# Kernel optimization log

Measured on AMD Instinct MI355X. Metric: run time of the kernel, lower is better.

## Reference

```python
import jax, jax.numpy as jnp
import numpy as np

WS = (7, 7, 7)          # window size (S, H, W)
NUM_HEADS = 6
DIM = 192
B_, NW = 128, 32        # total windows, windows per image (mask dim)
N = WS[0] * WS[1] * WS[2]  # 343 tokens per window


def _relative_position_index():
    # Faithful replica of the torch __init__ logic (incl. indexing='xy' and
    # the 3*W1-1 / 2*W1-1 multipliers).
    cs = np.arange(WS[0]); ch = np.arange(WS[1]); cw = np.arange(WS[2])
    coords = np.stack(np.meshgrid(cs, ch, cw, indexing='xy'))  # (3, Wh, Ws, Ww)
    cf = coords.reshape(3, -1)                                  # (3, N)
    rel = cf[:, :, None] - cf[:, None, :]                       # (3, N, N)
    rel = rel.transpose(1, 2, 0).astype(np.int64)               # (N, N, 3)
    rel[:, :, 0] += WS[0] - 1
    rel[:, :, 1] += WS[1] - 1
    rel[:, :, 2] += WS[2] - 1
    rel[:, :, 0] *= 3 * WS[1] - 1
    rel[:, :, 1] *= 2 * WS[1] - 1
    return rel.sum(-1)                                          # (N, N) int


def setup_inputs() -> dict:
    key = jax.random.key(0)
    ks = jax.random.split(key, 6)
    C = DIM
    x = jax.random.normal(ks[0], (B_, N, C), dtype=jnp.float32)
    mask = jax.random.normal(ks[1], (NW, N, N), dtype=jnp.float32)
    qkv_w = jax.random.normal(ks[2], (3 * C, C), dtype=jnp.float32) * 0.02
    qkv_b = jnp.zeros((3 * C,), dtype=jnp.float32)
    proj_w = jax.random.normal(ks[3], (C, C), dtype=jnp.float32) * 0.02
    proj_b = jnp.zeros((C,), dtype=jnp.float32)
    table_len = (2 * WS[0] - 1) * (2 * WS[1] - 1) * (2 * WS[2] - 1)
    rpb_table = jax.random.normal(ks[4], (table_len, NUM_HEADS), dtype=jnp.float32) * 0.02
    rel_index = jnp.asarray(_relative_position_index(), dtype=jnp.int32)
    return {"x": x, "mask": mask, "qkv_w": qkv_w, "qkv_b": qkv_b,
            "proj_w": proj_w, "proj_b": proj_b, "rpb_table": rpb_table,
            "rel_index": rel_index}


def reference(x, mask, qkv_w, qkv_b, proj_w, proj_b, rpb_table, rel_index):
    B, n, C = x.shape
    H = NUM_HEADS
    hd = C // H
    scale = hd ** (-0.5)
    qkv = x @ qkv_w.T + qkv_b                      # (B, N, 3C)
    qkv = qkv.reshape(B, n, 3, H, hd).transpose(2, 0, 3, 1, 4)  # (3, B, H, N, hd)
    q, k, v = qkv[0] * scale, qkv[1], qkv[2]
    attn = jnp.einsum('bhnd,bhmd->bhnm', q, k)     # (B, H, N, N)
    bias = rpb_table[rel_index.reshape(-1)].reshape(n, n, H)
    attn = attn + bias.transpose(2, 0, 1)[None]    # (B, H, N, N)
    nW = mask.shape[0]
    attn = attn.reshape(B // nW, nW, H, n, n) + mask[None, :, None]
    attn = jax.nn.softmax(attn.reshape(B, H, n, n), axis=-1)
    out = jnp.einsum('bhnm,bhmd->bhnd', attn, v)   # (B, H, N, hd)
    out = out.transpose(0, 2, 1, 3).reshape(B, n, C)
    return out @ proj_w.T + proj_b
```

## Files before the change

### kernel.cpp

```cpp
#include <hip/hip_runtime.h>
#include <hip/hip_fp16.h>
#include <hip/hip_bf16.h>
#include <stdint.h>

#define WN 343
#define NH 6
#define HD 32
#define CD 192
#define NB 128
#define NWM 32
#define BMROW 352
#define BMSLICE (11*16*BMROW)
#define BMKC (16*BMROW)
#define LOG2E 1.4426950408889634f
#define XTS 2064

typedef __attribute__((ext_vector_type(8))) short short8;
typedef __attribute__((ext_vector_type(4))) float f32x4;

__device__ __forceinline__ unsigned short f2bf(float f) {
  union { float f; uint32_t u; } v; v.f = f;
  uint32_t r = v.u + 0x7fffu + ((v.u >> 16) & 1u);
  return (unsigned short)(r >> 16);
}

__device__ __forceinline__ uint32_t pk2bf(float a, float b) {
  __hip_bfloat162 h = __float22bfloat162_rn(make_float2(a, b));
  return *(uint32_t*)&h;
}

__device__ __forceinline__ uint32_t pkh2(float a, float b) {
  __half2 h; h.x = __float2half(a); h.y = __float2half(b);
  return *(uint32_t*)&h;
}

typedef const __attribute__((address_space(1))) unsigned int* gas_ptr;
typedef __attribute__((address_space(3))) unsigned int* las_ptr;
__device__ __forceinline__ void gload16(const unsigned short* g, unsigned short* l) {
  __builtin_amdgcn_global_load_lds((gas_ptr)(const void*)g, (las_ptr)(void*)l, 16, 0, 0);
}

__device__ __forceinline__ void pipe_bar() {
  asm volatile("s_waitcnt vmcnt(0) lgkmcnt(0)" ::: "memory");
  __builtin_amdgcn_sched_barrier(0);
  __builtin_amdgcn_s_barrier();
  __builtin_amdgcn_sched_barrier(0);
}

__global__ __launch_bounds__(256) void prep_kernel(
    const float* __restrict__ wq, const float* __restrict__ wp,
    unsigned short* __restrict__ wqb, unsigned short* __restrict__ wpb,
    const int* __restrict__ rel, const float* __restrict__ rpb,
    const float* __restrict__ mask, uint32_t* __restrict__ bP,
    uint32_t* __restrict__ mP) {
  __shared__ float M[88][33];
  const int bid = blockIdx.x;
  const int tid = threadIdx.x;
  if (bid < 264) {
    const int h = bid / 44;
    const int rem = bid - h * 44;
    const int kc = rem >> 2;
    const int g = rem & 3;
    const int n0 = g * 88;
    const int k0 = kc * 32;
    for (int idx = tid; idx < 88 * 32; idx += 256) {
      int nl = idx >> 5, k = idx & 31;
      int n = n0 + nl;
      int nc = (n < WN) ? n : (WN - 1);
      M[nl][k] = (k0 + k < WN) ? rpb[rel[nc * WN + k0 + k] * NH + h] * LOG2E
                               : -30000.0f;
    }
    __syncthreads();
    uint32_t* outp = bP + (size_t)h * BMSLICE + (size_t)kc * BMKC;
    if (tid < 88) {
      const int nl = tid;
      const int n = n0 + nl;
#pragma unroll
      for (int quad = 0; quad < 4; ++quad) {
        uint4 o;
        o.x = pkh2(M[nl][quad * 8 + 0], M[nl][quad * 8 + 4]);
        o.y = pkh2(M[nl][quad * 8 + 1], M[nl][quad * 8 + 5]);
        o.z = pkh2(M[nl][quad * 8 + 2], M[nl][quad * 8 + 6]);
        o.w = pkh2(M[nl][quad * 8 + 3], M[nl][quad * 8 + 7]);
        *(uint4*)(outp + ((size_t)quad * 352 + n) * 4) = o;
      }
    }
    return;
  }
  int cb = bid - 264;
  if (cb < 352) {
    const int wdx = cb / 11;
    const int kc = cb - wdx * 11;
    const int k0 = kc * 32;
    const float* mw = mask + (size_t)wdx * (WN * WN);
    uint32_t* outp = mP + (size_t)wdx * BMSLICE + (size_t)kc * BMKC;
#pragma unroll
    for (int quad = 0; quad < 4; ++quad) {
      const int q8 = quad * 8;
#pragma unroll
      for (int j = 0; j < 2; ++j) {
        int n = tid + 256 * j;
        if (n < 352) {
          float v[8];
#pragma unroll
          for (int i = 0; i < 8; ++i) {
            int kk = k0 + q8 + i;
            v[i] = (n < WN && kk < WN) ? mw[n * WN + kk] * LOG2E : 0.0f;
          }
          uint4 o;
          o.x = pkh2(v[0], v[4]);
          o.y = pkh2(v[1], v[5]);
          o.z = pkh2(v[2], v[6]);
          o.w = pkh2(v[3], v[7]);
          *(uint4*)(outp + ((size_t)quad * 352 + n) * 4) = o;
        }
      }
    }
    return;
  }
  cb -= 352;
  if (cb < 54) {
    int g = cb * 256 + tid;
    int sk = g / 768; int rem = g - sk * 768;
    int row = rem >> 2; int cc = rem & 3;
    int s = sk / 6; int kt = sk - s * 6;
    int lch = cc ^ ((row >> 1) & 3);
    const float* src = wq + (size_t)(s * 192 + row) * CD + kt * 32 + lch * 8;
    f32x4 a = *(const f32x4*)src;
    f32x4 b = *(const f32x4*)(src + 4);
    union { short8 v8; uint32_t d[4]; } pk;
    pk.d[0] = pk2bf(a[0], a[1]);
    pk.d[1] = pk2bf(a[2], a[3]);
    pk.d[2] = pk2bf(b[0], b[1]);
    pk.d[3] = pk2bf(b[2], b[3]);
    *(short8*)(wqb + (size_t)g * 8) = pk.v8;
    return;
  }
  cb -= 54;
  int g = cb * 256 + tid;
  int kt = g / 768; int rem = g - kt * 768;
  int row = rem >> 2; int cc = rem & 3;
  int lch = cc ^ ((row >> 1) & 3);
  const float* src = wp + (size_t)row * CD + kt * 32 + lch * 8;
  f32x4 a = *(const f32x4*)src;
  f32x4 b = *(const f32x4*)(src + 4);
  union { short8 v8; uint32_t d[4]; } pk;
  pk.d[0] = pk2bf(a[0], a[1]);
  pk.d[1] = pk2bf(a[2], a[3]);
  pk.d[2] = pk2bf(b[0], b[1]);
  pk.d[3] = pk2bf(b[2], b[3]);
  *(short8*)(wpb + (size_t)g * 8) = pk.v8;
}

__global__ __launch_bounds__(256) void qkv_kernel(
    const float* __restrict__ x, const unsigned short* __restrict__ wqb,
    const float* __restrict__ bvec,
    unsigned short* __restrict__ qb, unsigned short* __restrict__ kb,
    unsigned short* __restrict__ vb) {
  __shared__ __align__(16) unsigned short SL[6 * XTS + 2 * 6144];
  unsigned short* B0 = SL + 6 * XTS;
  unsigned short* B1 = B0 + 6144;
  const int tid = threadIdx.x;
  const int wave = tid >> 6, lane = tid & 63;
  const int quad = lane >> 4, c = lane & 15;
  const int m0 = blockIdx.x * 64;
  const int chk = (quad ^ ((c >> 1) & 3)) * 8;

  auto WSTAGE = [&](unsigned short* buf, int s, int kt) {
    const unsigned short* gw = wqb + ((size_t)s * 6 + kt) * 6144 + tid * 8;
    unsigned short* lw = buf + (size_t)wave * 512;
    gload16(gw, lw);
    gload16(gw + 2048, lw + 2048);
    gload16(gw + 4096, lw + 4096);
  };

  WSTAGE(B0, 0, 0);
#pragma unroll
  for (int it = 0; it < 6; ++it) {
    int u = tid + 256 * it;
    int lrow = u / 24, c24 = u - lrow * 24;
    int kt = c24 >> 2, j = c24 & 3;
    const float* src = x + (size_t)(m0 + lrow) * CD + kt * 32 + j * 8;
    f32x4 a = *(const f32x4*)src;
    f32x4 b = *(const f32x4*)(src + 4);
    union { short8 v8; uint32_t d[4]; } pk;
    pk.d[0] = pk2bf(a[0], a[1]);
    pk.d[1] = pk2bf(a[2], a[3]);
    pk.d[2] = pk2bf(b[0], b[1]);
    pk.d[3] = pk2bf(b[2], b[3]);
    int cw = (j ^ ((lrow >> 1) & 3)) * 8;
    *(short8*)&SL[kt * XTS + lrow * 32 + cw] = pk.v8;
  }
  pipe_bar();

  const float qscale = 0.25503486f;
  f32x4 acc[12];
  unsigned short* Lh0 = B0;
  unsigned short* Lh1 = B0 + 2304;

  for (int s = 0; s < 3; ++s) {
#pragma unroll
    for (int j = 0; j < 12; ++j) acc[j] = (f32x4){0.f, 0.f, 0.f, 0.f};

    for (int kt = 0; kt < 6; ++kt) {
      unsigned short* cur = (kt & 1) ? B1 : B0;
      unsigned short* nxt = (kt & 1) ? B0 : B1;
      if (kt < 5) WSTAGE(nxt, s, kt + 1);
      const unsigned short* XLb = SL + kt * XTS;
      short8 af = *(const short8*)&XLb[(wave * 16 + c) * 32 + chk];
#pragma unroll
      for (int j = 0; j < 12; ++j) {
        short8 bfr = *(const short8*)&cur[(j * 16 + c) * 32 + chk];
        acc[j] = __builtin_amdgcn_mfma_f32_16x16x32_bf16(af, bfr, acc[j], 0, 0, 0);
      }
      pipe_bar();
    }

    unsigned short* dst = (s == 0) ? qb : ((s == 1) ? kb : vb);
    const float scl = (s == 0) ? qscale : 1.0f;
    const int n0 = s * 192;
    for (int hh = 0; hh < 3; ++hh) {
      __syncthreads();
#pragma unroll
      for (int jj = 0; jj < 4; ++jj) {
        int j = hh * 4 + jj;
        int hl = jj >> 1;
        int dd = (jj & 1) * 16 + c;
        float bn = bvec[n0 + j * 16 + c];
        unsigned short* L = hl ? Lh1 : Lh0;
#pragma unroll
        for (int r = 0; r < 4; ++r) {
          int m = wave * 16 + quad * 4 + r;
          L[m * 36 + dd] = f2bf((acc[j][r] + bn) * scl);
        }
      }
      __syncthreads();
      const int m = tid & 63;
      const int hl = (tid >> 6) & 1;
      const int half = tid >> 7;
      const int M = m0 + m;
      const int b = M / WN;
      const int tok = M - b * WN;
      const int h = hh * 2 + hl;
      const unsigned short* L = hl ? Lh1 : Lh0;
      unsigned short* drow = dst + (((size_t)b * NH + h) * WN + tok) * HD + half * 16;
      *(short8*)&drow[0] = *(const short8*)&L[m * 36 + half * 16];
      *(short8*)&drow[8] = *(const short8*)&L[m * 36 + half * 16 + 8];
    }
    if (s < 2) {
      __syncthreads();
      WSTAGE(B0, s + 1, 0);
      pipe_bar();
    }
  }
}

__global__ __launch_bounds__(512) void attn_kernel(
    const unsigned short* __restrict__ qb, const unsigned short* __restrict__ kb,
    const unsigned short* __restrict__ vb, const uint32_t* __restrict__ biasP,
    const uint32_t* __restrict__ maskP, unsigned short* __restrict__ ob) {
  __shared__ __align__(16) unsigned short Ks[352][40];
  __shared__ __align__(16) unsigned short Vt[HD][360];
  const int bid = blockIdx.x;
  const int job = (bid & 7) * 96 + (bid >> 3);
  const int wdx = job / 24;
  const int inner = job - wdx * 24;
  const int h = inner >> 2;
  const int b = (inner & 3) * 32 + wdx;
  const int tid = threadIdx.x;
  const int wave = tid >> 6, lane = tid & 63;
  const int quad = lane >> 4, c = lane & 15;
  const size_t base = ((size_t)b * NH + h) * (WN * HD);
  const unsigned short* q = qb + base;
  const unsigned short* k = kb + base;
  const unsigned short* v = vb + base;
  const uint32_t* bS = biasP + (size_t)h * BMSLICE;
  const uint32_t* mS = maskP + (size_t)wdx * BMSLICE;

  for (int t = tid; t < WN * 4; t += 512) {
    int r = t >> 2, ch = t & 3;
    int kk = r & 31;
    int row = (r & ~31) + 16 * ((kk >> 2) & 1) + 4 * (kk >> 3) + (kk & 3);
    *(short8*)&Ks[row][ch * 8] = *(const short8*)(k + r * HD + ch * 8);
  }
  for (int t = tid; t < 9 * 32; t += 512) {
    int kg = WN + (t >> 5);
    int kk = kg & 31;
    int row = (kg & ~31) + 16 * ((kk >> 2) & 1) + 4 * (kk >> 3) + (kk & 3);
    Ks[row][t & 31] = 0;
  }
  for (int t = tid; t < WN; t += 512) {
#pragma unroll
    for (int ch = 0; ch < 4; ++ch) {
      short8 vv = *(const short8*)(v + t * HD + ch * 8);
#pragma unroll
      for (int j = 0; j < 8; ++j) Vt[ch * 8 + j][t] = vv[j];
    }
  }
  for (int t = tid; t < 9 * 32; t += 512) {
    Vt[t & 31][WN + (t >> 5)] = 0;
  }
  __syncthreads();

  union { short8 v8; uint32_t d[4]; } on;
  on.d[0] = on.d[1] = on.d[2] = on.d[3] = 0x3F803F80u;

  for (int qt = wave; qt < 22; qt += 8) {
    const int q0 = qt * 16;
    int qr = q0 + c; if (qr > WN - 1) qr = WN - 1;
    const short8 qf = *(const short8*)(q + qr * HD + quad * 8);
    const uint32_t* bPtr = bS + ((size_t)quad * 352 + q0 + c) * 4;
    const uint32_t* mPtr = mS + ((size_t)quad * 352 + q0 + c) * 4;

    f32x4 o0 = (f32x4){0.f, 0.f, 0.f, 0.f};
    f32x4 o1 = (f32x4){0.f, 0.f, 0.f, 0.f};
    f32x4 accl = (f32x4){0.f, 0.f, 0.f, 0.f};
    uint4 bw = *(const uint4*)bPtr;
    uint4 mw = *(const uint4*)mPtr;
#pragma unroll 1
    for (int kc = 0; kc < 11; ++kc) {
      bPtr += BMKC; mPtr += BMKC;
      uint4 bwN = *(const uint4*)bPtr;
      uint4 mwN = *(const uint4*)mPtr;
      f32x4 cc0, cc1;
      {
        __half2 s2; float2 f;
        s2 = __hadd2(*(__half2*)&bw.x, *(__half2*)&mw.x);
        f = __half22float2(s2); cc0[0] = f.x; cc1[0] = f.y;
        s2 = __hadd2(*(__half2*)&bw.y, *(__half2*)&mw.y);
        f = __half22float2(s2); cc0[1] = f.x; cc1[1] = f.y;
        s2 = __hadd2(*(__half2*)&bw.z, *(__half2*)&mw.z);
        f = __half22float2(s2); cc0[2] = f.x; cc1[2] = f.y;
        s2 = __hadd2(*(__half2*)&bw.w, *(__half2*)&mw.w);
        f = __half22float2(s2); cc0[3] = f.x; cc1[3] = f.y;
      }
      const int k0 = kc * 32;
      short8 kf0 = *(const short8*)&Ks[k0 + c][quad * 8];
      short8 kf1 = *(const short8*)&Ks[k0 + 16 + c][quad * 8];
      __builtin_amdgcn_s_setprio(1);
      f32x4 s0 = __builtin_amdgcn_mfma_f32_16x16x32_bf16(kf0, qf, cc0, 0, 0, 0);
      f32x4 s1 = __builtin_amdgcn_mfma_f32_16x16x32_bf16(kf1, qf, cc1, 0, 0, 0);
      __builtin_amdgcn_s_setprio(0);
      float p0 = __builtin_amdgcn_exp2f(s0[0]), p1 = __builtin_amdgcn_exp2f(s0[1]);
      float p2 = __builtin_amdgcn_exp2f(s0[2]), p3 = __builtin_amdgcn_exp2f(s0[3]);
      float p4 = __builtin_amdgcn_exp2f(s1[0]), p5 = __builtin_amdgcn_exp2f(s1[1]);
      float p6 = __builtin_amdgcn_exp2f(s1[2]), p7 = __builtin_amdgcn_exp2f(s1[3]);
      union { short8 v8; uint32_t d[4]; } pf;
      pf.d[0] = pk2bf(p0, p1);
      pf.d[1] = pk2bf(p2, p3);
      pf.d[2] = pk2bf(p4, p5);
      pf.d[3] = pk2bf(p6, p7);
      short8 vf0 = *(const short8*)&Vt[c][k0 + quad * 8];
      short8 vf1 = *(const short8*)&Vt[16 + c][k0 + quad * 8];
      __builtin_amdgcn_s_setprio(1);
      o0 = __builtin_amdgcn_mfma_f32_16x16x32_bf16(pf.v8, vf0, o0, 0, 0, 0);
      o1 = __builtin_amdgcn_mfma_f32_16x16x32_bf16(pf.v8, vf1, o1, 0, 0, 0);
      accl = __builtin_amdgcn_mfma_f32_16x16x32_bf16(pf.v8, on.v8, accl, 0, 0, 0);
      __builtin_amdgcn_s_setprio(0);
      bw = bwN; mw = mwN;
    }

#pragma unroll
    for (int r = 0; r < 4; ++r) {
      int n = q0 + quad * 4 + r;
      if (n < WN) {
        float inv = 1.0f / accl[r];
        int M = b * WN + n;
        int rloc = M & 127;
        int xr2 = (rloc >> 1) & 3;
        size_t base2 = (((size_t)(M >> 7) * 6 + h) << 12) + rloc * 32;
        ob[base2 + (((c >> 3) ^ xr2) << 3) + (c & 7)] = f2bf(o0[r] * inv);
        ob[base2 + ((((c >> 3) | 2) ^ xr2) << 3) + (c & 7)] = f2bf(o1[r] * inv);
      }
    }
  }
}

__global__ __launch_bounds__(256) void proj_kernel(
    const unsigned short* __restrict__ obp, const unsigned short* __restrict__ wpb,
    const float* __restrict__ bvec, float* __restrict__ out) {
  __shared__ __align__(16) unsigned short SL[16384];
  const int tid = threadIdx.x;
  const int wave = tid >> 6, lane = tid & 63;
  const int quad = lane >> 4, c = lane & 15;
  const int m0 = blockIdx.x * 64;
  const int mb = blockIdx.x >> 1;
  const int r0 = (blockIdx.x & 1) * 64;
  const int chk = (quad ^ ((c >> 1) & 3)) * 8;

  f32x4 acc[12];
#pragma unroll
  for (int j = 0; j < 12; ++j) acc[j] = (f32x4){0.f, 0.f, 0.f, 0.f};

  auto STAGE = [&](unsigned short* buf, int kt) {
    const unsigned short* gx =
        obp + (((size_t)mb * 6 + kt) << 12) + r0 * 32 + tid * 8;
    const unsigned short* gw = wpb + (size_t)kt * 6144 + tid * 8;
    unsigned short* lx = buf + (size_t)wave * 512;
    unsigned short* lw = buf + 2048 + (size_t)wave * 512;
    gload16(gx, lx);
    gload16(gw, lw);
    gload16(gw + 2048, lw + 2048);
    gload16(gw + 4096, lw + 4096);
  };
  auto COMPUTE = [&](const unsigned short* buf) {
    const unsigned short* XLb = buf;
    const unsigned short* WLb = buf + 2048;
    short8 af = *(const short8*)&XLb[(wave * 16 + c) * 32 + chk];
#pragma unroll
    for (int j = 0; j < 12; ++j) {
      short8 bfr = *(const short8*)&WLb[(j * 16 + c) * 32 + chk];
      acc[j] = __builtin_amdgcn_mfma_f32_16x16x32_bf16(af, bfr, acc[j], 0, 0, 0);
    }
  };

  unsigned short* B0 = SL;
  unsigned short* B1 = SL + 8192;
  STAGE(B0, 0);
  pipe_bar();
#pragma unroll
  for (int p = 0; p < 3; ++p) {
    STAGE(B1, 2 * p + 1);
    COMPUTE(B0);
    pipe_bar();
    if (p < 2) STAGE(B0, 2 * p + 2);
    COMPUTE(B1);
    pipe_bar();
  }

#pragma unroll
  for (int j = 0; j < 12; ++j) {
    int col = j * 16 + c;
    float bn = bvec[col];
#pragma unroll
    for (int r = 0; r < 4; ++r) {
      int m = m0 + wave * 16 + quad * 4 + r;
      out[(size_t)m * CD + col] = acc[j][r] + bn;
    }
  }
}

extern "C" void kernel_launch(void* const* d_in, const int* in_sizes, int n_in,
                              void* d_out, int out_size, void* d_ws, size_t ws_size,
                              hipStream_t stream) {
  const float* x      = (const float*)d_in[0];
  const float* mask   = (const float*)d_in[1];
  const float* qkv_w  = (const float*)d_in[2];
  const float* qkv_b  = (const float*)d_in[3];
  const float* proj_w = (const float*)d_in[4];
  const float* proj_b = (const float*)d_in[5];
  const float* rpb    = (const float*)d_in[6];
  const int*   rel    = (const int*)d_in[7];
  float* out = (float*)d_out;

  char* ws = (char*)d_ws;
  uint32_t* biasP = (uint32_t*)ws;
  size_t off = 1486848;
  uint32_t* maskP = (uint32_t*)(ws + off); off += 7929856;
  unsigned short* qb = (unsigned short*)(ws + off); off += 16859136;
  unsigned short* kb = (unsigned short*)(ws + off); off += 16859136;
  unsigned short* vb = (unsigned short*)(ws + off); off += 16859136;
  unsigned short* wqb = (unsigned short*)(ws + off); off += 221184;
  unsigned short* wpb = (unsigned short*)(ws + off); off += 73728;
  unsigned short* obuf = (unsigned short*)(ws + off); off += 16859136;

  hipLaunchKernelGGL(prep_kernel, dim3(264 + 352 + 54 + 18), dim3(256),
                     0, stream,
                     qkv_w, proj_w, wqb, wpb, rel, rpb, mask, biasP, maskP);
  hipLaunchKernelGGL(qkv_kernel, dim3(686), dim3(256), 0, stream,
                     x, wqb, qkv_b, qb, kb, vb);
  hipLaunchKernelGGL(attn_kernel, dim3(NH * NB), dim3(512), 0, stream,
                     qb, kb, vb, biasP, maskP, obuf);
  hipLaunchKernelGGL(proj_kernel, dim3(686), dim3(256), 0, stream,
                     obuf, wpb, proj_b, out);
}
```

Measured before the change: 207.7 us.

## Fold bias, mask and proj-weight prep into the QKV GEMM launch

Splits the prep kernel so that only the QKV weight conversion runs first as a small kernel. The bias table, mask packing and projection weight conversion now run as extra blocks appended to the QKV GEMM grid, so they overlap with the GEMM instead of forming a serial stage. Mask block indices are also remapped so each group of eight consecutive blocks covers different windows. The cost is a larger combined kernel whose register and LDS budget is set by the GEMM path, applied to the prep blocks too.

```diff
diff --git a/kernel.cpp b/kernel.cpp
--- a/kernel.cpp
+++ b/kernel.cpp
@@ -47,18 +47,140 @@
   __builtin_amdgcn_sched_barrier(0);
 }
 
-__global__ __launch_bounds__(256) void prep_kernel(
-    const float* __restrict__ wq, const float* __restrict__ wp,
-    unsigned short* __restrict__ wqb, unsigned short* __restrict__ wpb,
+__global__ __launch_bounds__(256) void prep_w_kernel(
+    const float* __restrict__ wq, unsigned short* __restrict__ wqb) {
+  int g = blockIdx.x * 256 + threadIdx.x;
+  int sk = g / 768; int rem = g - sk * 768;
+  int row = rem >> 2; int cc = rem & 3;
+  int s = sk / 6; int kt = sk - s * 6;
+  int lch = cc ^ ((row >> 1) & 3);
+  const float* src = wq + (size_t)(s * 192 + row) * CD + kt * 32 + lch * 8;
+  f32x4 a = *(const f32x4*)src;
+  f32x4 b = *(const f32x4*)(src + 4);
+  union { short8 v8; uint32_t d[4]; } pk;
+  pk.d[0] = pk2bf(a[0], a[1]);
+  pk.d[1] = pk2bf(a[2], a[3]);
+  pk.d[2] = pk2bf(b[0], b[1]);
+  pk.d[3] = pk2bf(b[2], b[3]);
+  *(short8*)(wqb + (size_t)g * 8) = pk.v8;
+}
+
+__global__ __launch_bounds__(256) void qkv_kernel(
+    const float* __restrict__ x, const unsigned short* __restrict__ wqb,
+    const float* __restrict__ bvec,
+    unsigned short* __restrict__ qb, unsigned short* __restrict__ kb,
+    unsigned short* __restrict__ vb,
     const int* __restrict__ rel, const float* __restrict__ rpb,
     const float* __restrict__ mask, uint32_t* __restrict__ bP,
-    uint32_t* __restrict__ mP) {
-  __shared__ float M[88][33];
+    uint32_t* __restrict__ mP,
+    const float* __restrict__ wp, unsigned short* __restrict__ wpb) {
+  __shared__ __align__(16) unsigned short SL[6 * XTS + 2 * 6144];
   const int bid = blockIdx.x;
   const int tid = threadIdx.x;
-  if (bid < 264) {
-    const int h = bid / 44;
-    const int rem = bid - h * 44;
+
+  if (bid < 686) {
+    unsigned short* B0 = SL + 6 * XTS;
+    unsigned short* B1 = B0 + 6144;
+    const int wave = tid >> 6, lane = tid & 63;
+    const int quad = lane >> 4, c = lane & 15;
+    const int m0 = bid * 64;
+    const int chk = (quad ^ ((c >> 1) & 3)) * 8;
+
+    auto WSTAGE = [&](unsigned short* buf, int s, int kt) {
+      const unsigned short* gw = wqb + ((size_t)s * 6 + kt) * 6144 + tid * 8;
+      unsigned short* lw = buf + (size_t)wave * 512;
+      gload16(gw, lw);
+      gload16(gw + 2048, lw + 2048);
+      gload16(gw + 4096, lw + 4096);
+    };
+
+    WSTAGE(B0, 0, 0);
+#pragma unroll
+    for (int it = 0; it < 6; ++it) {
+      int u = tid + 256 * it;
+      int lrow = u / 24, c24 = u - lrow * 24;
+      int kt = c24 >> 2, j = c24 & 3;
+      const float* src = x + (size_t)(m0 + lrow) * CD + kt * 32 + j * 8;
+      f32x4 a = *(const f32x4*)src;
+      f32x4 b = *(const f32x4*)(src + 4);
+      union { short8 v8; uint32_t d[4]; } pk;
+      pk.d[0] = pk2bf(a[0], a[1]);
+      pk.d[1] = pk2bf(a[2], a[3]);
+      pk.d[2] = pk2bf(b[0], b[1]);
+      pk.d[3] = pk2bf(b[2], b[3]);
+      int cw = (j ^ ((lrow >> 1) & 3)) * 8;
+      *(short8*)&SL[kt * XTS + lrow * 32 + cw] = pk.v8;
+    }
+    pipe_bar();
+
+    const float qscale = 0.25503486f;
+    f32x4 acc[12];
+    unsigned short* Lh0 = B0;
+    unsigned short* Lh1 = B0 + 2304;
+
+    for (int s = 0; s < 3; ++s) {
+#pragma unroll
+      for (int j = 0; j < 12; ++j) acc[j] = (f32x4){0.f, 0.f, 0.f, 0.f};
+
+      for (int kt = 0; kt < 6; ++kt) {
+        unsigned short* cur = (kt & 1) ? B1 : B0;
+        unsigned short* nxt = (kt & 1) ? B0 : B1;
+        if (kt < 5) WSTAGE(nxt, s, kt + 1);
+        const unsigned short* XLb = SL + kt * XTS;
+        short8 af = *(const short8*)&XLb[(wave * 16 + c) * 32 + chk];
+#pragma unroll
+        for (int j = 0; j < 12; ++j) {
+          short8 bfr = *(const short8*)&cur[(j * 16 + c) * 32 + chk];
+          acc[j] = __builtin_amdgcn_mfma_f32_16x16x32_bf16(af, bfr, acc[j], 0, 0, 0);
+        }
+        pipe_bar();
+      }
+
+      unsigned short* dst = (s == 0) ? qb : ((s == 1) ? kb : vb);
+      const float scl = (s == 0) ? qscale : 1.0f;
+      const int n0 = s * 192;
+      for (int hh = 0; hh < 3; ++hh) {
+        __syncthreads();
+#pragma unroll
+        for (int jj = 0; jj < 4; ++jj) {
+          int j = hh * 4 + jj;
+          int hl = jj >> 1;
+          int dd = (jj & 1) * 16 + c;
+          float bn = bvec[n0 + j * 16 + c];
+          unsigned short* L = hl ? Lh1 : Lh0;
+#pragma unroll
+          for (int r = 0; r < 4; ++r) {
+            int m = wave * 16 + quad * 4 + r;
+            L[m * 36 + dd] = f2bf((acc[j][r] + bn) * scl);
+          }
+        }
+        __syncthreads();
+        const int m = tid & 63;
+        const int hl = (tid >> 6) & 1;
+        const int half = tid >> 7;
+        const int M = m0 + m;
+        const int b = M / WN;
+        const int tok = M - b * WN;
+        const int h = hh * 2 + hl;
+        const unsigned short* L = hl ? Lh1 : Lh0;
+        unsigned short* drow = dst + (((size_t)b * NH + h) * WN + tok) * HD + half * 16;
+        *(short8*)&drow[0] = *(const short8*)&L[m * 36 + half * 16];
+        *(short8*)&drow[8] = *(const short8*)&L[m * 36 + half * 16 + 8];
+      }
+      if (s < 2) {
+        __syncthreads();
+        WSTAGE(B0, s + 1, 0);
+        pipe_bar();
+      }
+    }
+    return;
+  }
+
+  int cb = bid - 686;
+  if (cb < 264) {
+    float (*M)[33] = (float (*)[33])&SL[0];
+    const int h = cb / 44;
+    const int rem = cb - h * 44;
     const int kc = rem >> 2;
     const int g = rem & 3;
     const int n0 = g * 88;
@@ -87,10 +209,12 @@
     }
     return;
   }
-  int cb = bid - 264;
+  cb -= 264;
   if (cb < 352) {
-    const int wdx = cb / 11;
-    const int kc = cb - wdx * 11;
+    const int g = bid & 7;
+    const int t = cb >> 3;
+    const int wdx = 4 * g + t / 11;
+    const int kc = t - 11 * (t / 11);
     const int k0 = kc * 32;
     const float* mw = mask + (size_t)wdx * (WN * WN);
     uint32_t* outp = mP + (size_t)wdx * BMSLICE + (size_t)kc * BMKC;
@@ -119,24 +243,6 @@
     return;
   }
   cb -= 352;
-  if (cb < 54) {
-    int g = cb * 256 + tid;
-    int sk = g / 768; int rem = g - sk * 768;
-    int row = rem >> 2; int cc = rem & 3;
-    int s = sk / 6; int kt = sk - s * 6;
-    int lch = cc ^ ((row >> 1) & 3);
-    const float* src = wq + (size_t)(s * 192 + row) * CD + kt * 32 + lch * 8;
-    f32x4 a = *(const f32x4*)src;
-    f32x4 b = *(const f32x4*)(src + 4);
-    union { short8 v8; uint32_t d[4]; } pk;
-    pk.d[0] = pk2bf(a[0], a[1]);
-    pk.d[1] = pk2bf(a[2], a[3]);
-    pk.d[2] = pk2bf(b[0], b[1]);
-    pk.d[3] = pk2bf(b[2], b[3]);
-    *(short8*)(wqb + (size_t)g * 8) = pk.v8;
-    return;
-  }
-  cb -= 54;
   int g = cb * 256 + tid;
   int kt = g / 768; int rem = g - kt * 768;
   int row = rem >> 2; int cc = rem & 3;
@@ -150,109 +256,6 @@
   pk.d[2] = pk2bf(b[0], b[1]);
   pk.d[3] = pk2bf(b[2], b[3]);
   *(short8*)(wpb + (size_t)g * 8) = pk.v8;
-}
-
-__global__ __launch_bounds__(256) void qkv_kernel(
-    const float* __restrict__ x, const unsigned short* __restrict__ wqb,
-    const float* __restrict__ bvec,
-    unsigned short* __restrict__ qb, unsigned short* __restrict__ kb,
-    unsigned short* __restrict__ vb) {
-  __shared__ __align__(16) unsigned short SL[6 * XTS + 2 * 6144];
-  unsigned short* B0 = SL + 6 * XTS;
-  unsigned short* B1 = B0 + 6144;
-  const int tid = threadIdx.x;
-  const int wave = tid >> 6, lane = tid & 63;
-  const int quad = lane >> 4, c = lane & 15;
-  const int m0 = blockIdx.x * 64;
-  const int chk = (quad ^ ((c >> 1) & 3)) * 8;
-
-  auto WSTAGE = [&](unsigned short* buf, int s, int kt) {
-    const unsigned short* gw = wqb + ((size_t)s * 6 + kt) * 6144 + tid * 8;
-    unsigned short* lw = buf + (size_t)wave * 512;
-    gload16(gw, lw);
-    gload16(gw + 2048, lw + 2048);
-    gload16(gw + 4096, lw + 4096);
-  };
-
-  WSTAGE(B0, 0, 0);
-#pragma unroll
-  for (int it = 0; it < 6; ++it) {
-    int u = tid + 256 * it;
-    int lrow = u / 24, c24 = u - lrow * 24;
-    int kt = c24 >> 2, j = c24 & 3;
-    const float* src = x + (size_t)(m0 + lrow) * CD + kt * 32 + j * 8;
-    f32x4 a = *(const f32x4*)src;
-    f32x4 b = *(const f32x4*)(src + 4);
-    union { short8 v8; uint32_t d[4]; } pk;
-    pk.d[0] = pk2bf(a[0], a[1]);
-    pk.d[1] = pk2bf(a[2], a[3]);
-    pk.d[2] = pk2bf(b[0], b[1]);
-    pk.d[3] = pk2bf(b[2], b[3]);
-    int cw = (j ^ ((lrow >> 1) & 3)) * 8;
-    *(short8*)&SL[kt * XTS + lrow * 32 + cw] = pk.v8;
-  }
-  pipe_bar();
-
-  const float qscale = 0.25503486f;
-  f32x4 acc[12];
-  unsigned short* Lh0 = B0;
-  unsigned short* Lh1 = B0 + 2304;
-
-  for (int s = 0; s < 3; ++s) {
-#pragma unroll
-    for (int j = 0; j < 12; ++j) acc[j] = (f32x4){0.f, 0.f, 0.f, 0.f};
-
-    for (int kt = 0; kt < 6; ++kt) {
-      unsigned short* cur = (kt & 1) ? B1 : B0;
-      unsigned short* nxt = (kt & 1) ? B0 : B1;
-      if (kt < 5) WSTAGE(nxt, s, kt + 1);
-      const unsigned short* XLb = SL + kt * XTS;
-      short8 af = *(const short8*)&XLb[(wave * 16 + c) * 32 + chk];
-#pragma unroll
-      for (int j = 0; j < 12; ++j) {
-        short8 bfr = *(const short8*)&cur[(j * 16 + c) * 32 + chk];
-        acc[j] = __builtin_amdgcn_mfma_f32_16x16x32_bf16(af, bfr, acc[j], 0, 0, 0);
-      }
-      pipe_bar();
-    }
-
-    unsigned short* dst = (s == 0) ? qb : ((s == 1) ? kb : vb);
-    const float scl = (s == 0) ? qscale : 1.0f;
-    const int n0 = s * 192;
-    for (int hh = 0; hh < 3; ++hh) {
-      __syncthreads();
-#pragma unroll
-      for (int jj = 0; jj < 4; ++jj) {
-        int j = hh * 4 + jj;
-        int hl = jj >> 1;
-        int dd = (jj & 1) * 16 + c;
-        float bn = bvec[n0 + j * 16 + c];
-        unsigned short* L = hl ? Lh1 : Lh0;
-#pragma unroll
-        for (int r = 0; r < 4; ++r) {
-          int m = wave * 16 + quad * 4 + r;
-          L[m * 36 + dd] = f2bf((acc[j][r] + bn) * scl);
-        }
-      }
-      __syncthreads();
-      const int m = tid & 63;
-      const int hl = (tid >> 6) & 1;
-      const int half = tid >> 7;
-      const int M = m0 + m;
-      const int b = M / WN;
-      const int tok = M - b * WN;
-      const int h = hh * 2 + hl;
-      const unsigned short* L = hl ? Lh1 : Lh0;
-      unsigned short* drow = dst + (((size_t)b * NH + h) * WN + tok) * HD + half * 16;
-      *(short8*)&drow[0] = *(const short8*)&L[m * 36 + half * 16];
-      *(short8*)&drow[8] = *(const short8*)&L[m * 36 + half * 16 + 8];
-    }
-    if (s < 2) {
-      __syncthreads();
-      WSTAGE(B0, s + 1, 0);
-      pipe_bar();
-    }
-  }
 }
 
 __global__ __launch_bounds__(512) void attn_kernel(
@@ -464,11 +467,11 @@
   unsigned short* wpb = (unsigned short*)(ws + off); off += 73728;
   unsigned short* obuf = (unsigned short*)(ws + off); off += 16859136;
 
-  hipLaunchKernelGGL(prep_kernel, dim3(264 + 352 + 54 + 18), dim3(256),
-                     0, stream,
-                     qkv_w, proj_w, wqb, wpb, rel, rpb, mask, biasP, maskP);
-  hipLaunchKernelGGL(qkv_kernel, dim3(686), dim3(256), 0, stream,
-                     x, wqb, qkv_b, qb, kb, vb);
+  hipLaunchKernelGGL(prep_w_kernel, dim3(54), dim3(256), 0, stream,
+                     qkv_w, wqb);
+  hipLaunchKernelGGL(qkv_kernel, dim3(686 + 264 + 352 + 18), dim3(256), 0, stream,
+                     x, wqb, qkv_b, qb, kb, vb,
+                     rel, rpb, mask, biasP, maskP, proj_w, wpb);
   hipLaunchKernelGGL(attn_kernel, dim3(NH * NB), dim3(512), 0, stream,
                      qb, kb, vb, biasP, maskP, obuf);
   hipLaunchKernelGGL(proj_kernel, dim3(686), dim3(256), 0, stream,
```

New measurement: 191.5 us. 1.08x faster.
